# Optimization experiments

Hardware: AMD Instinct MI355X
Metric: run time of the kernel (lower is better)

## Reference

```python
import jax, jax.numpy as jnp
import numpy as np

N, OBS, ENC, ACT, K = 16384, 512, 512, 64, 8
ALPHA = 1.0


def setup_inputs() -> dict:
    key = jax.random.key(0)
    ks = jax.random.split(key, 8)
    s = 0.05  # keep activations/logits well-scaled
    return {
        "X1": jax.random.normal(ks[0], (N, OBS), jnp.float32),
        "X0": jax.random.normal(ks[1], (N, OBS), jnp.float32),
        "U": jax.random.normal(ks[2], (N, ACT), jnp.float32),
        "W_enc": jax.random.normal(ks[3], (ENC, OBS), jnp.float32) * s,
        "A_all": jax.random.normal(ks[4], (K, ENC, ENC), jnp.float32) * s,
        "B_rest": jax.random.normal(ks[5], (K - 1, ACT, ENC), jnp.float32) * s,
        "C_w": jax.random.normal(ks[6], (K, ENC), jnp.float32) * s,
        "C_b": jax.random.normal(ks[7], (K,), jnp.float32) * s,
    }


def reference(X1, X0, U, W_enc, A_all, B_rest, C_w, C_b):
    enc_dim = W_enc.shape[0]
    act_dim = U.shape[1]
    k = A_all.shape[0]
    # encoder: bias-free linear
    X1e = X1 @ W_enc.T  # [N, enc]
    X0e = X0 @ W_enc.T  # [N, enc]
    # gating: argmax of linear classifier C
    inds = jnp.argmax(X0e @ C_w.T + C_b, axis=1)  # [N]
    # expert 0 uses fixed B0 = eye(enc)[:act, :]; experts 1..k-1 learned
    B0 = jnp.eye(enc_dim, dtype=X0.dtype)[:act_dim]  # [act, enc]
    B_all = jnp.concatenate([B0[None], B_rest], axis=0)  # [k, act, enc]
    # per-expert predictions for every row (nn.Linear: x @ W.T -> einsum over input dim h)
    preds = jnp.einsum('nh,keh->kne', X0e, A_all) + jnp.einsum('na,kae->kne', U, B_all)
    # squared error per (expert, row), then select each row's routed expert
    sq = jnp.sum((X1e[None, :, :] - preds) ** 2, axis=-1)  # [k, N]
    onehot = jax.nn.one_hot(inds, k, dtype=sq.dtype)  # [N, k]
    loss = ALPHA * jnp.sum(sq * onehot.T)
    return loss / (enc_dim * X1.shape[0])
```

## Files before the change

kernel.cpp:

```cpp
#include <hip/hip_runtime.h>

#define NROWS 16384
#define OBSD 512
#define ENCD 512
#define ACTD 64
#define KEXP 8

typedef __attribute__((ext_vector_type(8))) short bf16x8;
typedef __attribute__((ext_vector_type(4))) float f32x4;
typedef __attribute__((address_space(3))) unsigned char lds_byte;
typedef __attribute__((address_space(1))) unsigned char glb_byte;

__device__ __forceinline__ unsigned short f2bf(float f) {
  unsigned int u = __float_as_uint(f);
  u = (u + 0x7FFFu + ((u >> 16) & 1u)) >> 16;
  return (unsigned short)u;
}
__device__ __forceinline__ unsigned int cvtpk(float lo, float hi) {
  unsigned int r;
  asm("v_cvt_pk_bf16_f32 %0, %1, %2" : "=v"(r) : "v"(lo), "v"(hi));
  return r;
}
__device__ __forceinline__ void gload_lds16(const unsigned short* g, unsigned short* l) {
  __builtin_amdgcn_global_load_lds((const glb_byte*)g, (lds_byte*)l, 16, 0, 0);
}

__global__ __launch_bounds__(256) void gt_k(
    const float* __restrict__ W, const float* __restrict__ Cw,
    float* __restrict__ GT, float* __restrict__ loss,
    int* __restrict__ counts, int* __restrict__ cursor) {
  const int b = blockIdx.x, tid = threadIdx.x;
  if (b == 0) {
    if (tid == 0) *loss = 0.f;
    if (tid < KEXP) { counts[tid] = 0; cursor[tid] = 0; }
  }
  __shared__ float red[4][64];
  int e = b >> 3, o0 = (b & 7) * 64;
  int o = tid & 63, hg = tid >> 6;
  float s = 0.f;
#pragma unroll 8
  for (int h = hg * 128; h < hg * 128 + 128; h++)
    s += Cw[e * ENCD + h] * W[(size_t)h * OBSD + o0 + o];
  red[hg][o] = s;
  __syncthreads();
  if (tid < 64)
    GT[(o0 + tid) * KEXP + e] = red[0][tid] + red[1][tid] + red[2][tid] + red[3][tid];
}

__global__ __launch_bounds__(256) void fused_prep_k(
    const float* __restrict__ X0, const float* __restrict__ X1,
    const float* __restrict__ U, const float* __restrict__ W,
    const float* __restrict__ Aall, const float* __restrict__ Brest,
    const float* __restrict__ GT, const float* __restrict__ Cb,
    unsigned short* __restrict__ X0bf, unsigned short* __restrict__ X1bf,
    unsigned short* __restrict__ Ubf, unsigned short* __restrict__ Wbf,
    unsigned short* __restrict__ AbfN, unsigned short* __restrict__ BfTN,
    int* __restrict__ inds, int* __restrict__ counts) {
  const int b = blockIdx.x, tid = threadIdx.x;
  if (b < 512) {
    __shared__ int lhist[KEXP];
    if (tid < KEXP) lhist[tid] = 0;
    __syncthreads();
    const int lane = tid & 63, w = tid >> 6;
    float g[8][8];
    const float* gp = GT + lane * 8 * KEXP;
#pragma unroll
    for (int j = 0; j < 8; j++) {
      float4 lo = *(const float4*)(gp + j * KEXP);
      float4 hi = *(const float4*)(gp + j * KEXP + 4);
      g[j][0] = lo.x; g[j][1] = lo.y; g[j][2] = lo.z; g[j][3] = lo.w;
      g[j][4] = hi.x; g[j][5] = hi.y; g[j][6] = hi.z; g[j][7] = hi.w;
    }
    float cb[KEXP];
#pragma unroll
    for (int e = 0; e < KEXP; e++) cb[e] = Cb[e];
#pragma unroll 2
    for (int r = 0; r < 8; r++) {
      const int n = b * 32 + w * 8 + r;
      const float4* xr = (const float4*)(X0 + (size_t)n * OBSD + lane * 8);
      float4 x = xr[0], y = xr[1];
      float xv[8] = {x.x, x.y, x.z, x.w, y.x, y.y, y.z, y.w};
      float acc[KEXP] = {};
#pragma unroll
      for (int j = 0; j < 8; j++)
#pragma unroll
        for (int e = 0; e < KEXP; e++) acc[e] += xv[j] * g[j][e];
      uint4 rr = {cvtpk(x.x, x.y), cvtpk(x.z, x.w), cvtpk(y.x, y.y), cvtpk(y.z, y.w)};
      *(uint4*)&X0bf[(size_t)n * OBSD + lane * 8] = rr;
#pragma unroll
      for (int e = 0; e < KEXP; e++) {
#pragma unroll
        for (int off = 32; off > 0; off >>= 1) acc[e] += __shfl_xor(acc[e], off, 64);
      }
      if (lane == 0) {
        int best = 0;
        float bv = acc[0] + cb[0];
#pragma unroll
        for (int e = 1; e < KEXP; e++) {
          float v = acc[e] + cb[e];
          if (v > bv) { bv = v; best = e; }
        }
        inds[n] = best;
        atomicAdd(&lhist[best], 1);
      }
    }
    __syncthreads();
    if (tid < KEXP) atomicAdd(&counts[tid], lhist[tid]);
    return;
  }
  if (b < 4608) {
    size_t i = ((size_t)(b - 512) * 256 + tid) * 8;
    const float4* s4 = (const float4*)(X1 + i);
    float4 a = s4[0], c = s4[1];
    uint4 r = {cvtpk(a.x, a.y), cvtpk(a.z, a.w), cvtpk(c.x, c.y), cvtpk(c.z, c.w)};
    *(uint4*)&X1bf[i] = r;
    return;
  }
  if (b < 4664) {
    __shared__ float tile[64][65];
    int t = b - 4608;
    int k = (t >> 3);
    int e0 = (t & 7) * 64;
    const float* src = Brest + (size_t)k * ACTD * ENCD + e0;
#pragma unroll
    for (int j = 0; j < 16; j++) {
      int idx = j * 256 + tid;
      int a = idx >> 6, e = idx & 63;
      tile[a][e] = src[(size_t)a * ENCD + e];
    }
    __syncthreads();
    unsigned short* dst = BfTN + ((size_t)(k + 1) * ENCD + e0) * ACTD;
#pragma unroll
    for (int j = 0; j < 16; j++) {
      int idx = j * 256 + tid;
      int e = idx >> 6, a = idx & 63;
      dst[(size_t)e * ACTD + a] = f2bf(-tile[a][e]);
    }
    return;
  }
  if (b == 4664) {
    for (int j = 0; j < 16; j++) {
      int i8 = j * 256 + tid;
      int e = i8 >> 3, a0 = (i8 & 7) * 8;
      unsigned int w0 = 0, w1 = 0, w2 = 0, w3 = 0;
      if (e >= a0 && e < a0 + 8) {
        unsigned int bits = 0xBF80u << ((e & 1) * 16);
        if ((e - a0) >> 1 == 0) w0 = bits;
        else if ((e - a0) >> 1 == 1) w1 = bits;
        else if ((e - a0) >> 1 == 2) w2 = bits;
        else w3 = bits;
      }
      uint4 v = {w0, w1, w2, w3};
      *(uint4*)&BfTN[(size_t)i8 * 8] = v;
    }
    return;
  }
  int cb2 = b - 4665;
  if (cb2 < 1024) {
    size_t i = (size_t)cb2 * 256 + tid;
    float4 v = ((const float4*)U)[i];
    uint2 r = {cvtpk(v.x, v.y), cvtpk(v.z, v.w)};
    *(uint2*)&Ubf[i * 4] = r;
  } else if (cb2 < 1280) {
    size_t i = (size_t)(cb2 - 1024) * 256 + tid;
    float4 v = ((const float4*)W)[i];
    uint2 r = {cvtpk(v.x, v.y), cvtpk(v.z, v.w)};
    *(uint2*)&Wbf[i * 4] = r;
  } else {
    size_t i = (size_t)(cb2 - 1280) * 256 + tid;
    float4 v = ((const float4*)Aall)[i];
    uint2 r = {cvtpk(-v.x, -v.y), cvtpk(-v.z, -v.w)};
    *(uint2*)&AbfN[i * 4] = r;
  }
}

__global__ void prefix_k(const int* __restrict__ counts, int* __restrict__ cursor,
                         int* __restrict__ starts) {
  if (threadIdx.x == 0 && blockIdx.x == 0) {
    int s = 0;
    for (int k = 0; k < KEXP; k++) { starts[k] = s; cursor[k] = s; s += counts[k]; }
    starts[KEXP] = s;
  }
}

__global__ __launch_bounds__(256, 2) void enc_scatter_k(
    const unsigned short* __restrict__ X0bf, const unsigned short* __restrict__ Wbf,
    unsigned short* __restrict__ X0e, const int* __restrict__ inds,
    int* __restrict__ cursor, int* __restrict__ rowlist) {
  if (blockIdx.x >= 512) {
    __shared__ int lhist[KEXP], lbase[KEXP];
    const int tid = threadIdx.x;
    if (tid < KEXP) lhist[tid] = 0;
    __syncthreads();
    const int n = (blockIdx.x - 512) * 256 + tid;
    const int r = inds[n];
    const int lpos = atomicAdd(&lhist[r], 1);
    __syncthreads();
    if (tid < KEXP) lbase[tid] = atomicAdd(&cursor[tid], lhist[tid]);
    __syncthreads();
    rowlist[lbase[r] + lpos] = n;
    return;
  }
  __shared__ unsigned short As[128 * 64];
  __shared__ unsigned short Bs[128 * 64];
  const int tid = threadIdx.x;
  const int bid = blockIdx.x;
  const int lid = (bid & 7) * 64 + (bid >> 3);
  const int col0 = (lid & 3) * 128;
  const int row0 = (lid >> 2) * 128;

  const int lane = tid & 63, w = tid >> 6;
  const int wr = w >> 1, wc = w & 1;
  const int srow8 = tid >> 3;
  const int lslot = ((tid & 7) ^ (srow8 & 7)) * 8;
  const int ldsoff = tid * 8;
  const int r15 = lane & 15;
  const int qk = lane >> 4;
  const int rsw = r15 & 7;
  const int arow = wr * 64 + r15;
  const int brow = wc * 64 + r15;

  f32x4 acc[4][4] = {};
  for (int k0 = 0; k0 < OBSD; k0 += 64) {
#pragma unroll
    for (int j = 0; j < 4; j++) {
      int row = j * 32 + srow8;
      gload_lds16(X0bf + (size_t)(row0 + row) * OBSD + k0 + lslot, &As[j * 2048 + ldsoff]);
      gload_lds16(Wbf + (size_t)(col0 + row) * OBSD + k0 + lslot, &Bs[j * 2048 + ldsoff]);
    }
    __syncthreads();
#pragma unroll
    for (int kk = 0; kk < 2; kk++) {
      const int ps = ((kk * 4 + qk) ^ rsw) * 8;
      bf16x8 af[4], bfr[4];
#pragma unroll
      for (int m = 0; m < 4; m++) af[m] = *(const bf16x8*)&As[(arow + m * 16) * 64 + ps];
#pragma unroll
      for (int n = 0; n < 4; n++) bfr[n] = *(const bf16x8*)&Bs[(brow + n * 16) * 64 + ps];
#pragma unroll
      for (int m = 0; m < 4; m++)
#pragma unroll
        for (int n = 0; n < 4; n++)
          acc[m][n] = __builtin_amdgcn_mfma_f32_16x16x32_bf16(bfr[n], af[m], acc[m][n], 0, 0, 0);
    }
    __syncthreads();
  }
#pragma unroll
  for (int m = 0; m < 4; m++) {
    int rowg = row0 + wr * 64 + m * 16 + r15;
#pragma unroll
    for (int n = 0; n < 4; n++) {
      int colg = col0 + wc * 64 + n * 16 + qk * 4;
      uint2 v = {cvtpk(acc[m][n][0], acc[m][n][1]), cvtpk(acc[m][n][2], acc[m][n][3])};
      *(uint2*)&X0e[(size_t)rowg * ENCD + colg] = v;
    }
  }
}

__global__ __launch_bounds__(256, 2) void grouped_mfma_k(
    const unsigned short* __restrict__ X1bf, const unsigned short* __restrict__ X0ebf,
    const unsigned short* __restrict__ Wbf, const unsigned short* __restrict__ Ubf,
    const unsigned short* __restrict__ AbfN, const unsigned short* __restrict__ BfTN,
    const int* __restrict__ rowlist, const int* __restrict__ starts,
    float* __restrict__ loss) {
  const int tid = threadIdx.x;
  const int bid = blockIdx.x;
  const int lid = (bid & 7) * 512 + (bid >> 3);
  const int k = lid >> 9;
  const int rem = lid & 511;
  const int col0 = (rem & 3) * 128;
  const int tile = rem >> 2;

  const int start = starts[k];
  const int cnt = starts[k + 1] - start;
  if (tile * 128 >= cnt) return;

  __shared__ unsigned short As[128 * 64];
  __shared__ unsigned short Bs[128 * 64];
  __shared__ int ridx[128];
  __shared__ float red[4];

  if (tid < 128) {
    int p = tile * 128 + tid;
    ridx[tid] = rowlist[start + (p < cnt ? p : 0)];
  }
  __syncthreads();

  const int lane = tid & 63, w = tid >> 6;
  const int wr = w >> 1, wc = w & 1;
  const int srow8 = tid >> 3;
  const int lslot = ((tid & 7) ^ (srow8 & 7)) * 8;
  const int ldsoff = tid * 8;
  const int r15 = lane & 15;
  const int qk = lane >> 4;
  const int rsw = r15 & 7;
  const int arow = wr * 64 + r15;
  const int brow = wc * 64 + r15;
  int rnj[4];
#pragma unroll
  for (int j = 0; j < 4; j++) rnj[j] = ridx[j * 32 + srow8];

  const unsigned short* AkN = AbfN + (size_t)k * ENCD * ENCD;
  const unsigned short* BfTkN = BfTN + (size_t)k * ENCD * ACTD;

  f32x4 acc[4][4] = {};
#define GROUPED_COMPUTE()                                                            \
  do {                                                                               \
    __syncthreads();                                                                 \
    _Pragma("unroll") for (int kk = 0; kk < 2; kk++) {                               \
      const int ps = ((kk * 4 + qk) ^ rsw) * 8;                                      \
      bf16x8 af[4], bfr[4];                                                          \
      _Pragma("unroll") for (int m = 0; m < 4; m++)                                  \
          af[m] = *(const bf16x8*)&As[(arow + m * 16) * 64 + ps];                    \
      _Pragma("unroll") for (int n = 0; n < 4; n++)                                  \
          bfr[n] = *(const bf16x8*)&Bs[(brow + n * 16) * 64 + ps];                   \
      _Pragma("unroll") for (int m = 0; m < 4; m++)                                  \
          _Pragma("unroll") for (int n = 0; n < 4; n++)                              \
              acc[m][n] = __builtin_amdgcn_mfma_f32_16x16x32_bf16(bfr[n], af[m],     \
                                                                  acc[m][n], 0, 0, 0); \
    }                                                                                \
    __syncthreads();                                                                 \
  } while (0)

  for (int k0 = 0; k0 < ENCD; k0 += 64) {
#pragma unroll
    for (int j = 0; j < 4; j++) {
      int row = j * 32 + srow8;
      gload_lds16(X1bf + (size_t)rnj[j] * OBSD + k0 + lslot, &As[j * 2048 + ldsoff]);
      gload_lds16(Wbf + (size_t)(col0 + row) * OBSD + k0 + lslot, &Bs[j * 2048 + ldsoff]);
    }
    GROUPED_COMPUTE();
  }
  for (int k0 = 0; k0 < ENCD; k0 += 64) {
#pragma unroll
    for (int j = 0; j < 4; j++) {
      int row = j * 32 + srow8;
      gload_lds16(X0ebf + (size_t)rnj[j] * ENCD + k0 + lslot, &As[j * 2048 + ldsoff]);
      gload_lds16(AkN + (size_t)(col0 + row) * ENCD + k0 + lslot, &Bs[j * 2048 + ldsoff]);
    }
    GROUPED_COMPUTE();
  }
  {
#pragma unroll
    for (int j = 0; j < 4; j++) {
      int row = j * 32 + srow8;
      gload_lds16(Ubf + (size_t)rnj[j] * ACTD + lslot, &As[j * 2048 + ldsoff]);
      gload_lds16(BfTkN + (size_t)(col0 + row) * ACTD + lslot, &Bs[j * 2048 + ldsoff]);
    }
    GROUPED_COMPUTE();
  }
#undef GROUPED_COMPUTE

  float sq = 0.f;
#pragma unroll
  for (int m = 0; m < 4; m++) {
    int lr = wr * 64 + m * 16 + r15;
    if (tile * 128 + lr < cnt) {
#pragma unroll
      for (int n = 0; n < 4; n++)
        sq += acc[m][n][0] * acc[m][n][0] + acc[m][n][1] * acc[m][n][1] +
              acc[m][n][2] * acc[m][n][2] + acc[m][n][3] * acc[m][n][3];
    }
  }
#pragma unroll
  for (int off = 32; off > 0; off >>= 1) sq += __shfl_xor(sq, off, 64);
  if (lane == 0) red[w] = sq;
  __syncthreads();
  if (tid == 0) atomicAdd(loss, red[0] + red[1] + red[2] + red[3]);
}

__global__ void finalize_k(const float* __restrict__ loss, float* __restrict__ out) {
  if (threadIdx.x == 0 && blockIdx.x == 0)
    out[0] = loss[0] * (1.0f / ((float)ENCD * (float)NROWS));
}

extern "C" void kernel_launch(void* const* d_in, const int* in_sizes, int n_in,
                              void* d_out, int out_size, void* d_ws, size_t ws_size,
                              hipStream_t stream) {
  const float* X1 = (const float*)d_in[0];
  const float* X0 = (const float*)d_in[1];
  const float* U = (const float*)d_in[2];
  const float* W = (const float*)d_in[3];
  const float* Aall = (const float*)d_in[4];
  const float* Brest = (const float*)d_in[5];
  const float* Cw = (const float*)d_in[6];
  const float* Cb = (const float*)d_in[7];
  float* out = (float*)d_out;

  char* p = (char*)d_ws;
  auto alloc = [&](size_t bytes) { char* r = p; p += (bytes + 255) & ~(size_t)255; return r; };
  unsigned short* X1bf = (unsigned short*)alloc((size_t)NROWS * OBSD * 2);
  unsigned short* X0bf = (unsigned short*)alloc((size_t)NROWS * OBSD * 2);
  unsigned short* Ubf = (unsigned short*)alloc((size_t)NROWS * ACTD * 2);
  unsigned short* Wbf = (unsigned short*)alloc((size_t)ENCD * OBSD * 2);
  unsigned short* AbfN = (unsigned short*)alloc((size_t)KEXP * ENCD * ENCD * 2);
  unsigned short* BfTN = (unsigned short*)alloc((size_t)KEXP * ENCD * ACTD * 2);
  unsigned short* X0ebf = (unsigned short*)alloc((size_t)NROWS * ENCD * 2);
  float* GT = (float*)alloc(KEXP * OBSD * 4);
  float* loss = (float*)alloc(256);
  int* inds = (int*)alloc(NROWS * 4);
  int* rowlist = (int*)alloc(NROWS * 4);
  int* counts = (int*)alloc(64);
  int* cursor = (int*)alloc(64);
  int* starts = (int*)alloc(64);

  gt_k<<<64, 256, 0, stream>>>(W, Cw, GT, loss, counts, cursor);
  fused_prep_k<<<7993, 256, 0, stream>>>(X0, X1, U, W, Aall, Brest, GT, Cb,
                                         X0bf, X1bf, Ubf, Wbf, AbfN, BfTN,
                                         inds, counts);
  prefix_k<<<1, 1, 0, stream>>>(counts, cursor, starts);
  enc_scatter_k<<<576, 256, 0, stream>>>(X0bf, Wbf, X0ebf, inds, cursor, rowlist);
  grouped_mfma_k<<<4096, 256, 0, stream>>>(X1bf, X0ebf, Wbf, Ubf, AbfN, BfTN,
                                           rowlist, starts, loss);
  finalize_k<<<1, 64, 0, stream>>>(loss, out);
}
```

Before: 83.73 us.

## Double-buffer LDS tiles in grouped MFMA kernel and drop prefix launch

The grouped expert GEMM now uses two LDS buffers and a single flattened 17-step loop. It issues the next tile's global-to-LDS loads before computing on the current tile, so load latency overlaps MFMA work. The separate single-thread prefix-sum kernel is removed: expert starts are computed inline from counts in both the scatter and grouped kernels. This saves one launch but doubles LDS use per block, which may limit occupancy.

```diff
diff --git a/kernel.cpp b/kernel.cpp
--- a/kernel.cpp
+++ b/kernel.cpp
@@ -174,23 +174,22 @@
   }
 }
 
-__global__ void prefix_k(const int* __restrict__ counts, int* __restrict__ cursor,
-                         int* __restrict__ starts) {
-  if (threadIdx.x == 0 && blockIdx.x == 0) {
-    int s = 0;
-    for (int k = 0; k < KEXP; k++) { starts[k] = s; cursor[k] = s; s += counts[k]; }
-    starts[KEXP] = s;
-  }
-}
-
 __global__ __launch_bounds__(256, 2) void enc_scatter_k(
     const unsigned short* __restrict__ X0bf, const unsigned short* __restrict__ Wbf,
     unsigned short* __restrict__ X0e, const int* __restrict__ inds,
-    int* __restrict__ cursor, int* __restrict__ rowlist) {
+    const int* __restrict__ counts, int* __restrict__ cursor,
+    int* __restrict__ rowlist) {
   if (blockIdx.x >= 512) {
-    __shared__ int lhist[KEXP], lbase[KEXP];
+    __shared__ int lhist[KEXP], lbase[KEXP], sstart[KEXP];
     const int tid = threadIdx.x;
-    if (tid < KEXP) lhist[tid] = 0;
+    if (tid < KEXP) {
+      lhist[tid] = 0;
+      int s = 0;
+      for (int j = 0; j < KEXP; j++) {
+        if (j == tid) sstart[tid] = s;
+        s += counts[j];
+      }
+    }
     __syncthreads();
     const int n = (blockIdx.x - 512) * 256 + tid;
     const int r = inds[n];
@@ -198,7 +197,7 @@
     __syncthreads();
     if (tid < KEXP) lbase[tid] = atomicAdd(&cursor[tid], lhist[tid]);
     __syncthreads();
-    rowlist[lbase[r] + lpos] = n;
+    rowlist[sstart[r] + lbase[r] + lpos] = n;
     return;
   }
   __shared__ unsigned short As[128 * 64];
@@ -261,7 +260,7 @@
     const unsigned short* __restrict__ X1bf, const unsigned short* __restrict__ X0ebf,
     const unsigned short* __restrict__ Wbf, const unsigned short* __restrict__ Ubf,
     const unsigned short* __restrict__ AbfN, const unsigned short* __restrict__ BfTN,
-    const int* __restrict__ rowlist, const int* __restrict__ starts,
+    const int* __restrict__ rowlist, const int* __restrict__ counts,
     float* __restrict__ loss) {
   const int tid = threadIdx.x;
   const int bid = blockIdx.x;
@@ -271,12 +270,17 @@
   const int col0 = (rem & 3) * 128;
   const int tile = rem >> 2;
 
-  const int start = starts[k];
-  const int cnt = starts[k + 1] - start;
+  int start = 0, cnt = 0;
+#pragma unroll
+  for (int j = 0; j < KEXP; j++) {
+    int c = counts[j];
+    if (j < k) start += c;
+    if (j == k) cnt = c;
+  }
   if (tile * 128 >= cnt) return;
 
-  __shared__ unsigned short As[128 * 64];
-  __shared__ unsigned short Bs[128 * 64];
+  __shared__ unsigned short As[2][128 * 64];
+  __shared__ unsigned short Bs[2][128 * 64];
   __shared__ int ridx[128];
   __shared__ float red[4];
 
@@ -303,53 +307,66 @@
   const unsigned short* AkN = AbfN + (size_t)k * ENCD * ENCD;
   const unsigned short* BfTkN = BfTN + (size_t)k * ENCD * ACTD;
 
+  auto stage = [&](int t, int buf) {
+    unsigned short* as = &As[buf][0];
+    unsigned short* bs = &Bs[buf][0];
+    if (t < 8) {
+      int k0 = t * 64;
+#pragma unroll
+      for (int j = 0; j < 4; j++) {
+        int row = j * 32 + srow8;
+        gload_lds16(X1bf + (size_t)rnj[j] * OBSD + k0 + lslot, &as[j * 2048 + ldsoff]);
+        gload_lds16(Wbf + (size_t)(col0 + row) * OBSD + k0 + lslot, &bs[j * 2048 + ldsoff]);
+      }
+    } else if (t < 16) {
+      int k0 = (t - 8) * 64;
+#pragma unroll
+      for (int j = 0; j < 4; j++) {
+        int row = j * 32 + srow8;
+        gload_lds16(X0ebf + (size_t)rnj[j] * ENCD + k0 + lslot, &as[j * 2048 + ldsoff]);
+        gload_lds16(AkN + (size_t)(col0 + row) * ENCD + k0 + lslot, &bs[j * 2048 + ldsoff]);
+      }
+    } else {
+#pragma unroll
+      for (int j = 0; j < 4; j++) {
+        int row = j * 32 + srow8;
+        gload_lds16(Ubf + (size_t)rnj[j] * ACTD + lslot, &as[j * 2048 + ldsoff]);
+        gload_lds16(BfTkN + (size_t)(col0 + row) * ACTD + lslot, &bs[j * 2048 + ldsoff]);
+      }
+    }
+  };
+
   f32x4 acc[4][4] = {};
-#define GROUPED_COMPUTE()                                                            \
-  do {                                                                               \
-    __syncthreads();                                                                 \
-    _Pragma("unroll") for (int kk = 0; kk < 2; kk++) {                               \
-      const int ps = ((kk * 4 + qk) ^ rsw) * 8;                                      \
-      bf16x8 af[4], bfr[4];                                                          \
-      _Pragma("unroll") for (int m = 0; m < 4; m++)                                  \
-          af[m] = *(const bf16x8*)&As[(arow + m * 16) * 64 + ps];                    \
-      _Pragma("unroll") for (int n = 0; n < 4; n++)                                  \
-          bfr[n] = *(const bf16x8*)&Bs[(brow + n * 16) * 64 + ps];                   \
-      _Pragma("unroll") for (int m = 0; m < 4; m++)                                  \
-          _Pragma("unroll") for (int n = 0; n < 4; n++)                              \
-              acc[m][n] = __builtin_amdgcn_mfma_f32_16x16x32_bf16(bfr[n], af[m],     \
-                                                                  acc[m][n], 0, 0, 0); \
-    }                                                                                \
-    __syncthreads();                                                                 \
-  } while (0)
-
-  for (int k0 = 0; k0 < ENCD; k0 += 64) {
-#pragma unroll
-    for (int j = 0; j < 4; j++) {
-      int row = j * 32 + srow8;
-      gload_lds16(X1bf + (size_t)rnj[j] * OBSD + k0 + lslot, &As[j * 2048 + ldsoff]);
-      gload_lds16(Wbf + (size_t)(col0 + row) * OBSD + k0 + lslot, &Bs[j * 2048 + ldsoff]);
-    }
-    GROUPED_COMPUTE();
-  }
-  for (int k0 = 0; k0 < ENCD; k0 += 64) {
-#pragma unroll
-    for (int j = 0; j < 4; j++) {
-      int row = j * 32 + srow8;
-      gload_lds16(X0ebf + (size_t)rnj[j] * ENCD + k0 + lslot, &As[j * 2048 + ldsoff]);
-      gload_lds16(AkN + (size_t)(col0 + row) * ENCD + k0 + lslot, &Bs[j * 2048 + ldsoff]);
-    }
-    GROUPED_COMPUTE();
-  }
-  {
-#pragma unroll
-    for (int j = 0; j < 4; j++) {
-      int row = j * 32 + srow8;
-      gload_lds16(Ubf + (size_t)rnj[j] * ACTD + lslot, &As[j * 2048 + ldsoff]);
-      gload_lds16(BfTkN + (size_t)(col0 + row) * ACTD + lslot, &Bs[j * 2048 + ldsoff]);
-    }
-    GROUPED_COMPUTE();
-  }
-#undef GROUPED_COMPUTE
+  auto compute = [&](int buf) {
+    const unsigned short* as = &As[buf][0];
+    const unsigned short* bs = &Bs[buf][0];
+#pragma unroll
+    for (int kk = 0; kk < 2; kk++) {
+      const int ps = ((kk * 4 + qk) ^ rsw) * 8;
+      bf16x8 af[4], bfr[4];
+#pragma unroll
+      for (int m = 0; m < 4; m++) af[m] = *(const bf16x8*)&as[(arow + m * 16) * 64 + ps];
+#pragma unroll
+      for (int n = 0; n < 4; n++) bfr[n] = *(const bf16x8*)&bs[(brow + n * 16) * 64 + ps];
+#pragma unroll
+      for (int m = 0; m < 4; m++)
+#pragma unroll
+        for (int n = 0; n < 4; n++)
+          acc[m][n] = __builtin_amdgcn_mfma_f32_16x16x32_bf16(bfr[n], af[m], acc[m][n], 0, 0, 0);
+    }
+  };
+
+  stage(0, 0);
+  asm volatile("s_waitcnt vmcnt(0)" ::: "memory");
+  __syncthreads();
+#pragma unroll 1
+  for (int t = 0; t < 17; ++t) {
+    const int cur = t & 1;
+    if (t < 16) stage(t + 1, cur ^ 1);
+    compute(cur);
+    asm volatile("s_waitcnt vmcnt(0)" ::: "memory");
+    __syncthreads();
+  }
 
   float sq = 0.f;
 #pragma unroll
@@ -402,15 +419,14 @@
   int* rowlist = (int*)alloc(NROWS * 4);
   int* counts = (int*)alloc(64);
   int* cursor = (int*)alloc(64);
-  int* starts = (int*)alloc(64);
 
   gt_k<<<64, 256, 0, stream>>>(W, Cw, GT, loss, counts, cursor);
   fused_prep_k<<<7993, 256, 0, stream>>>(X0, X1, U, W, Aall, Brest, GT, Cb,
                                          X0bf, X1bf, Ubf, Wbf, AbfN, BfTN,
                                          inds, counts);
-  prefix_k<<<1, 1, 0, stream>>>(counts, cursor, starts);
-  enc_scatter_k<<<576, 256, 0, stream>>>(X0bf, Wbf, X0ebf, inds, cursor, rowlist);
+  enc_scatter_k<<<576, 256, 0, stream>>>(X0bf, Wbf, X0ebf, inds, counts,
+                                         cursor, rowlist);
   grouped_mfma_k<<<4096, 256, 0, stream>>>(X1bf, X0ebf, Wbf, Ubf, AbfN, BfTN,
-                                           rowlist, starts, loss);
+                                           rowlist, counts, loss);
   finalize_k<<<1, 64, 0, stream>>>(loss, out);
 }
```

Result: slower. 95.19 us (+13.7%).

## Fold encoder into expert matrices via per-expert A_k·W product, drop X0e GEMM

Applied to the files above, without the earlier changes.

Instead of encoding every X0 row (a 16384x512x512 GEMM) and then multiplying by each expert's A_k, precompute M_k = A_k·W for all 8 experts (8x512x512x512) and apply M_k directly to bf16 X0 in the grouped kernel. This removes the X0e intermediate write/read and replaces the large encoder GEMM with a smaller weight-only product. It also drops the prefix_k launch by computing starts from counts inline, and adds a W transpose stage to the prep kernel. The extra bf16 rounding of M_k changes numerics slightly.

```diff
diff --git a/kernel.cpp b/kernel.cpp
--- a/kernel.cpp
+++ b/kernel.cpp
@@ -55,7 +55,8 @@
     unsigned short* __restrict__ X0bf, unsigned short* __restrict__ X1bf,
     unsigned short* __restrict__ Ubf, unsigned short* __restrict__ Wbf,
     unsigned short* __restrict__ AbfN, unsigned short* __restrict__ BfTN,
-    int* __restrict__ inds, int* __restrict__ counts) {
+    unsigned short* __restrict__ WbfT, int* __restrict__ inds,
+    int* __restrict__ counts) {
   const int b = blockIdx.x, tid = threadIdx.x;
   if (b < 512) {
     __shared__ int lhist[KEXP];
@@ -155,59 +156,80 @@
     }
     return;
   }
-  int cb2 = b - 4665;
-  if (cb2 < 1024) {
-    size_t i = (size_t)cb2 * 256 + tid;
-    float4 v = ((const float4*)U)[i];
-    uint2 r = {cvtpk(v.x, v.y), cvtpk(v.z, v.w)};
-    *(uint2*)&Ubf[i * 4] = r;
-  } else if (cb2 < 1280) {
-    size_t i = (size_t)(cb2 - 1024) * 256 + tid;
-    float4 v = ((const float4*)W)[i];
-    uint2 r = {cvtpk(v.x, v.y), cvtpk(v.z, v.w)};
-    *(uint2*)&Wbf[i * 4] = r;
-  } else {
-    size_t i = (size_t)(cb2 - 1280) * 256 + tid;
-    float4 v = ((const float4*)Aall)[i];
-    uint2 r = {cvtpk(-v.x, -v.y), cvtpk(-v.z, -v.w)};
-    *(uint2*)&AbfN[i * 4] = r;
-  }
-}
-
-__global__ void prefix_k(const int* __restrict__ counts, int* __restrict__ cursor,
-                         int* __restrict__ starts) {
-  if (threadIdx.x == 0 && blockIdx.x == 0) {
-    int s = 0;
-    for (int k = 0; k < KEXP; k++) { starts[k] = s; cursor[k] = s; s += counts[k]; }
-    starts[KEXP] = s;
-  }
-}
-
-__global__ __launch_bounds__(256, 2) void enc_scatter_k(
-    const unsigned short* __restrict__ X0bf, const unsigned short* __restrict__ Wbf,
-    unsigned short* __restrict__ X0e, const int* __restrict__ inds,
-    int* __restrict__ cursor, int* __restrict__ rowlist) {
-  if (blockIdx.x >= 512) {
-    __shared__ int lhist[KEXP], lbase[KEXP];
+  if (b < 7993) {
+    int cb2 = b - 4665;
+    if (cb2 < 1024) {
+      size_t i = (size_t)cb2 * 256 + tid;
+      float4 v = ((const float4*)U)[i];
+      uint2 r = {cvtpk(v.x, v.y), cvtpk(v.z, v.w)};
+      *(uint2*)&Ubf[i * 4] = r;
+    } else if (cb2 < 1280) {
+      size_t i = (size_t)(cb2 - 1024) * 256 + tid;
+      float4 v = ((const float4*)W)[i];
+      uint2 r = {cvtpk(v.x, v.y), cvtpk(v.z, v.w)};
+      *(uint2*)&Wbf[i * 4] = r;
+    } else {
+      size_t i = (size_t)(cb2 - 1280) * 256 + tid;
+      float4 v = ((const float4*)Aall)[i];
+      uint2 r = {cvtpk(-v.x, -v.y), cvtpk(-v.z, -v.w)};
+      *(uint2*)&AbfN[i * 4] = r;
+    }
+    return;
+  }
+  {
+    __shared__ float tile[64][65];
+    int t = b - 7993;
+    int h0 = (t >> 3) * 64, o0 = (t & 7) * 64;
+#pragma unroll
+    for (int j = 0; j < 16; j++) {
+      int idx = j * 256 + tid;
+      int a = idx >> 6, e = idx & 63;
+      tile[a][e] = W[(size_t)(h0 + a) * OBSD + o0 + e];
+    }
+    __syncthreads();
+#pragma unroll
+    for (int j = 0; j < 16; j++) {
+      int idx = j * 256 + tid;
+      int e = idx >> 6, a = idx & 63;
+      WbfT[(size_t)(o0 + e) * OBSD + h0 + a] = f2bf(tile[a][e]);
+    }
+  }
+}
+
+__global__ __launch_bounds__(256, 2) void scatmgemm_k(
+    const int* __restrict__ inds, const int* __restrict__ counts,
+    int* __restrict__ cursor, int* __restrict__ rowlist,
+    const unsigned short* __restrict__ AbfN, const unsigned short* __restrict__ WbfT,
+    unsigned short* __restrict__ MN) {
+  if (blockIdx.x < 64) {
+    __shared__ int lhist[KEXP], lbase[KEXP], sstart[KEXP];
     const int tid = threadIdx.x;
-    if (tid < KEXP) lhist[tid] = 0;
-    __syncthreads();
-    const int n = (blockIdx.x - 512) * 256 + tid;
+    if (tid < KEXP) {
+      lhist[tid] = 0;
+      int s = 0;
+      for (int j = 0; j < KEXP; j++) {
+        if (j == tid) sstart[tid] = s;
+        s += counts[j];
+      }
+    }
+    __syncthreads();
+    const int n = blockIdx.x * 256 + tid;
     const int r = inds[n];
     const int lpos = atomicAdd(&lhist[r], 1);
     __syncthreads();
     if (tid < KEXP) lbase[tid] = atomicAdd(&cursor[tid], lhist[tid]);
     __syncthreads();
-    rowlist[lbase[r] + lpos] = n;
+    rowlist[sstart[r] + lbase[r] + lpos] = n;
     return;
   }
   __shared__ unsigned short As[128 * 64];
   __shared__ unsigned short Bs[128 * 64];
   const int tid = threadIdx.x;
-  const int bid = blockIdx.x;
-  const int lid = (bid & 7) * 64 + (bid >> 3);
-  const int col0 = (lid & 3) * 128;
-  const int row0 = (lid >> 2) * 128;
+  const int t = blockIdx.x - 64;
+  const int k = t >> 4;
+  const int rem = t & 15;
+  const int row0 = (rem >> 2) * 128;
+  const int col0 = (rem & 3) * 128;
 
   const int lane = tid & 63, w = tid >> 6;
   const int wr = w >> 1, wc = w & 1;
@@ -219,14 +241,15 @@
   const int rsw = r15 & 7;
   const int arow = wr * 64 + r15;
   const int brow = wc * 64 + r15;
+  const unsigned short* Ak = AbfN + (size_t)k * ENCD * ENCD;
 
   f32x4 acc[4][4] = {};
-  for (int k0 = 0; k0 < OBSD; k0 += 64) {
+  for (int k0 = 0; k0 < ENCD; k0 += 64) {
 #pragma unroll
     for (int j = 0; j < 4; j++) {
       int row = j * 32 + srow8;
-      gload_lds16(X0bf + (size_t)(row0 + row) * OBSD + k0 + lslot, &As[j * 2048 + ldsoff]);
-      gload_lds16(Wbf + (size_t)(col0 + row) * OBSD + k0 + lslot, &Bs[j * 2048 + ldsoff]);
+      gload_lds16(Ak + (size_t)(row0 + row) * ENCD + k0 + lslot, &As[j * 2048 + ldsoff]);
+      gload_lds16(WbfT + (size_t)(col0 + row) * OBSD + k0 + lslot, &Bs[j * 2048 + ldsoff]);
     }
     __syncthreads();
 #pragma unroll
@@ -245,6 +268,7 @@
     }
     __syncthreads();
   }
+  unsigned short* Mk = MN + (size_t)k * ENCD * OBSD;
 #pragma unroll
   for (int m = 0; m < 4; m++) {
     int rowg = row0 + wr * 64 + m * 16 + r15;
@@ -252,16 +276,16 @@
     for (int n = 0; n < 4; n++) {
       int colg = col0 + wc * 64 + n * 16 + qk * 4;
       uint2 v = {cvtpk(acc[m][n][0], acc[m][n][1]), cvtpk(acc[m][n][2], acc[m][n][3])};
-      *(uint2*)&X0e[(size_t)rowg * ENCD + colg] = v;
+      *(uint2*)&Mk[(size_t)rowg * OBSD + colg] = v;
     }
   }
 }
 
 __global__ __launch_bounds__(256, 2) void grouped_mfma_k(
-    const unsigned short* __restrict__ X1bf, const unsigned short* __restrict__ X0ebf,
+    const unsigned short* __restrict__ X1bf, const unsigned short* __restrict__ X0bf,
     const unsigned short* __restrict__ Wbf, const unsigned short* __restrict__ Ubf,
-    const unsigned short* __restrict__ AbfN, const unsigned short* __restrict__ BfTN,
-    const int* __restrict__ rowlist, const int* __restrict__ starts,
+    const unsigned short* __restrict__ MN, const unsigned short* __restrict__ BfTN,
+    const int* __restrict__ rowlist, const int* __restrict__ counts,
     float* __restrict__ loss) {
   const int tid = threadIdx.x;
   const int bid = blockIdx.x;
@@ -271,8 +295,13 @@
   const int col0 = (rem & 3) * 128;
   const int tile = rem >> 2;
 
-  const int start = starts[k];
-  const int cnt = starts[k + 1] - start;
+  int start = 0, cnt = 0;
+#pragma unroll
+  for (int j = 0; j < KEXP; j++) {
+    int c = counts[j];
+    if (j < k) start += c;
+    if (j == k) cnt = c;
+  }
   if (tile * 128 >= cnt) return;
 
   __shared__ unsigned short As[128 * 64];
@@ -300,7 +329,7 @@
 #pragma unroll
   for (int j = 0; j < 4; j++) rnj[j] = ridx[j * 32 + srow8];
 
-  const unsigned short* AkN = AbfN + (size_t)k * ENCD * ENCD;
+  const unsigned short* MkN = MN + (size_t)k * ENCD * OBSD;
   const unsigned short* BfTkN = BfTN + (size_t)k * ENCD * ACTD;
 
   f32x4 acc[4][4] = {};
@@ -322,7 +351,7 @@
     __syncthreads();                                                                 \
   } while (0)
 
-  for (int k0 = 0; k0 < ENCD; k0 += 64) {
+  for (int k0 = 0; k0 < OBSD; k0 += 64) {
 #pragma unroll
     for (int j = 0; j < 4; j++) {
       int row = j * 32 + srow8;
@@ -331,12 +360,12 @@
     }
     GROUPED_COMPUTE();
   }
-  for (int k0 = 0; k0 < ENCD; k0 += 64) {
+  for (int k0 = 0; k0 < OBSD; k0 += 64) {
 #pragma unroll
     for (int j = 0; j < 4; j++) {
       int row = j * 32 + srow8;
-      gload_lds16(X0ebf + (size_t)rnj[j] * ENCD + k0 + lslot, &As[j * 2048 + ldsoff]);
-      gload_lds16(AkN + (size_t)(col0 + row) * ENCD + k0 + lslot, &Bs[j * 2048 + ldsoff]);
+      gload_lds16(X0bf + (size_t)rnj[j] * OBSD + k0 + lslot, &As[j * 2048 + ldsoff]);
+      gload_lds16(MkN + (size_t)(col0 + row) * OBSD + k0 + lslot, &Bs[j * 2048 + ldsoff]);
     }
     GROUPED_COMPUTE();
   }
@@ -395,22 +424,22 @@
   unsigned short* Wbf = (unsigned short*)alloc((size_t)ENCD * OBSD * 2);
   unsigned short* AbfN = (unsigned short*)alloc((size_t)KEXP * ENCD * ENCD * 2);
   unsigned short* BfTN = (unsigned short*)alloc((size_t)KEXP * ENCD * ACTD * 2);
-  unsigned short* X0ebf = (unsigned short*)alloc((size_t)NROWS * ENCD * 2);
+  unsigned short* WbfT = (unsigned short*)alloc((size_t)OBSD * ENCD * 2);
+  unsigned short* MN = (unsigned short*)alloc((size_t)KEXP * ENCD * OBSD * 2);
   float* GT = (float*)alloc(KEXP * OBSD * 4);
   float* loss = (float*)alloc(256);
   int* inds = (int*)alloc(NROWS * 4);
   int* rowlist = (int*)alloc(NROWS * 4);
   int* counts = (int*)alloc(64);
   int* cursor = (int*)alloc(64);
-  int* starts = (int*)alloc(64);
 
   gt_k<<<64, 256, 0, stream>>>(W, Cw, GT, loss, counts, cursor);
-  fused_prep_k<<<7993, 256, 0, stream>>>(X0, X1, U, W, Aall, Brest, GT, Cb,
+  fused_prep_k<<<8057, 256, 0, stream>>>(X0, X1, U, W, Aall, Brest, GT, Cb,
                                          X0bf, X1bf, Ubf, Wbf, AbfN, BfTN,
-                                         inds, counts);
-  prefix_k<<<1, 1, 0, stream>>>(counts, cursor, starts);
-  enc_scatter_k<<<576, 256, 0, stream>>>(X0bf, Wbf, X0ebf, inds, cursor, rowlist);
-  grouped_mfma_k<<<4096, 256, 0, stream>>>(X1bf, X0ebf, Wbf, Ubf, AbfN, BfTN,
-                                           rowlist, starts, loss);
+                                         WbfT, inds, counts);
+  scatmgemm_k<<<192, 256, 0, stream>>>(inds, counts, cursor, rowlist,
+                                       AbfN, WbfT, MN);
+  grouped_mfma_k<<<4096, 256, 0, stream>>>(X1bf, X0bf, Wbf, Ubf, MN, BfTN,
+                                           rowlist, counts, loss);
   finalize_k<<<1, 64, 0, stream>>>(loss, out);
 }
```

New measurement: 79.07 us. 1.06x faster.
